# Kernel optimization log

Hardware: AMD Instinct MI355X
Metric: run time of the kernel (lower is better)

## Reference

```python
import jax, jax.numpy as jnp
import numpy as np

# Static problem dims (match input_specs / init_kwargs)
B, NQ, C, H = 2, 900, 256, 8
HGT, WID = 64, 64            # single-scale feature map (input_spatial_shapes = [[64, 64]])
N = HGT * WID                # 4096 keys
DH = C // H                  # head dim 32
RPE_HID = 512
STRIDE = 16                  # feature_stride


def setup_inputs() -> dict:
    key = jax.random.key(0)
    ks = jax.random.split(key, 24)
    p = lambda k, shape: jax.random.normal(k, shape, jnp.float32) * 0.02
    # reference boxes (cx, cy, w, h) in pixel coords of a 1024x1024 image
    ref = jax.random.uniform(ks[0], (B, NQ, 1, 4), jnp.float32)
    ref = jnp.concatenate([ref[..., :2] * (WID * STRIDE), ref[..., 2:] * 128.0], axis=-1)
    return {
        "vggt_features": jnp.zeros((1,), jnp.float32),  # unused by forward (kept for signature fidelity)
        "query": jax.random.normal(ks[1], (B, NQ, C), jnp.float32),
        "reference_2d": ref,
        "k_input_flatten": jax.random.normal(ks[2], (B, N, C), jnp.float32),
        "v_input_flatten": jax.random.normal(ks[3], (B, N, C), jnp.float32),
        "input_spatial_shapes": jnp.array([[HGT, WID]], jnp.int32),
        "input_padding_mask": jnp.zeros((B, N), jnp.bool_),
        # cpb_mlp1 (x) and cpb_mlp2 (y): Linear(2,512)+ReLU+Linear(512,H,no bias); stored as [in,out]
        "W1x": p(ks[4], (2, RPE_HID)), "b1x": jnp.zeros((RPE_HID,), jnp.float32), "W2x": p(ks[5], (RPE_HID, H)),
        "W1y": p(ks[6], (2, RPE_HID)), "b1y": jnp.zeros((RPE_HID,), jnp.float32), "W2y": p(ks[7], (RPE_HID, H)),
        "Wq": p(ks[8], (C, C)), "bq": jnp.zeros((C,), jnp.float32),
        "Wk": p(ks[9], (C, C)), "bk": jnp.zeros((C,), jnp.float32),
        "Wv": p(ks[10], (C, C)), "bv": jnp.zeros((C,), jnp.float32),
        "Wp": p(ks[11], (C, C)), "bp": jnp.zeros((C,), jnp.float32),
    }


def _mlp(d, W1, b1, W2):
    return jax.nn.relu(d @ W1 + b1) @ W2


def reference(vggt_features, query, reference_2d, k_input_flatten, v_input_flatten,
              input_spatial_shapes, input_padding_mask,
              W1x, b1x, W2x, W1y, b1y, W2y, Wq, bq, Wk, bk, Wv, bv, Wp, bp):
    h, w = HGT, WID  # static (input_spatial_shapes[0] == [HGT, WID])
    scale = DH ** -0.5
    # cxcywh -> xyxy: [B, NQ, 1, 4]
    xyxy = jnp.concatenate([reference_2d[..., :2] - reference_2d[..., 2:] / 2,
                            reference_2d[..., :2] + reference_2d[..., 2:] / 2], axis=-1)
    # pixel-center grid coords (linspace(0.5, w-0.5, w) * stride)
    pos_x = ((jnp.arange(w, dtype=jnp.float32) + 0.5) * STRIDE)[None, None, :, None]
    pos_y = ((jnp.arange(h, dtype=jnp.float32) + 0.5) * STRIDE)[None, None, :, None]
    delta_x = xyxy[..., 0::2] - pos_x  # [B, NQ, w, 2]  (x1, x2 rel. to columns)
    delta_y = xyxy[..., 1::2] - pos_y  # [B, NQ, h, 2]  (y1, y2 rel. to rows)
    rpe_x = _mlp(delta_x, W1x, b1x, W2x)  # [B, NQ, w, H]
    rpe_y = _mlp(delta_y, W1y, b1y, W2y)  # [B, NQ, h, H]
    # broadcast add over (row, col) then flatten spatial -> [B, H, NQ, N]
    rpe = (rpe_x[:, :, None] + rpe_y[:, :, :, None]).reshape(B, NQ, h * w, H).transpose(0, 3, 1, 2)
    q = (query @ Wq + bq).reshape(B, NQ, H, DH).transpose(0, 2, 1, 3) * scale  # [B,H,NQ,DH]
    k = (k_input_flatten @ Wk + bk).reshape(B, N, H, DH).transpose(0, 2, 1, 3)  # [B,H,N,DH]
    v = (v_input_flatten @ Wv + bv).reshape(B, N, H, DH).transpose(0, 2, 1, 3)  # [B,H,N,DH]
    attn = jnp.einsum('bhqd,bhkd->bhqk', q, k) + rpe
    attn = attn + input_padding_mask[:, None, None, :].astype(attn.dtype) * (-100.0)
    # torch.clip_ to finfo(min,max) is an identity on finite values; softmax follows
    attn = jax.nn.softmax(attn, axis=-1)
    x = jnp.einsum('bhqk,bhkd->bhqd', attn, v).transpose(0, 2, 1, 3).reshape(B, NQ, C)
    return x @ Wp + bp
```

## Files before the change

### kernel.cpp

```cpp
#include <hip/hip_runtime.h>
#include <hip/hip_bf16.h>
#include <cmath>

#define B_ 2
#define NQ_ 900
#define N_ 4096
#define LOG2E 1.4426950408889634f

typedef __attribute__((ext_vector_type(4))) float f32x4;
typedef __attribute__((ext_vector_type(8))) short s16x8;
typedef __attribute__((ext_vector_type(8))) _Float16 f16x8;

__device__ inline short f2bf(float x) {
    union { __hip_bfloat16 b; short s; } u;
    u.b = __float2bfloat16(x);
    return u.s;
}
__device__ inline short f2h(float x) {
    _Float16 h = (_Float16)x;
    return __builtin_bit_cast(short, h);
}

template <int CTRL>
__device__ inline float dppf(float x) {
    int xi = __builtin_bit_cast(int, x);
    int r = __builtin_amdgcn_update_dpp(xi, xi, CTRL, 0xF, 0xF, true);
    return __builtin_bit_cast(float, r);
}
__device__ inline float rowmax16(float v) {
    v = fmaxf(v, dppf<0x121>(v));
    v = fmaxf(v, dppf<0x122>(v));
    v = fmaxf(v, dppf<0x124>(v));
    v = fmaxf(v, dppf<0x128>(v));
    return v;
}
__device__ inline float rowsum16(float v) {
    v += dppf<0x121>(v);
    v += dppf<0x122>(v);
    v += dppf<0x124>(v);
    v += dppf<0x128>(v);
    return v;
}

__global__ __launch_bounds__(256) void proj_kernel(
    const float* __restrict__ query, const float* __restrict__ kin,
    const float* __restrict__ vin,
    const float* __restrict__ Wq, const float* __restrict__ Wk,
    const float* __restrict__ Wv,
    const float* __restrict__ bqv, const float* __restrict__ bkv,
    const float* __restrict__ bvv,
    unsigned short* __restrict__ qbf, unsigned short* __restrict__ kbf,
    unsigned short* __restrict__ vbf, float qscale)
{
    const int mtx = blockIdx.z;
    const float* X = mtx == 0 ? query : mtx == 1 ? kin : vin;
    const float* W = mtx == 0 ? Wq : mtx == 1 ? Wk : Wv;
    const float* bias = mtx == 0 ? bqv : mtx == 1 ? bkv : bvv;
    unsigned short* Y = mtx == 0 ? qbf : mtx == 1 ? kbf : vbf;
    const int M = mtx == 0 ? 1800 : 8192;
    const int m0 = blockIdx.x * 64;
    if (m0 >= M) return;
    const float alpha = mtx == 0 ? qscale : 1.0f;
    const int rows_per_b = mtx == 0 ? 900 : 4096;
    const int ROWS = mtx == 0 ? 960 : 4096;

    __shared__ short Ab[16384];
    __shared__ short Bb[16384];
    const int tid = threadIdx.x;
    const int w = tid >> 6, l = tid & 63, quad = l >> 4, l15 = l & 15;
    const int wq = tid & 3, mm = tid >> 2;

    {
        const bool valid = (m0 + mm) < M;
        const float* xr = X + (size_t)(m0 + mm) * 256;
        #pragma unroll
        for (int it = 0; it < 8; ++it) {
            int g2 = it * 4 + wq;
            float4 a0 = make_float4(0.f, 0.f, 0.f, 0.f), a1 = a0;
            if (valid) {
                a0 = *(const float4*)(xr + g2 * 8);
                a1 = *(const float4*)(xr + g2 * 8 + 4);
            }
            uint4 pk;
            pk.x = (unsigned)(unsigned short)f2bf(a0.x) | ((unsigned)(unsigned short)f2bf(a0.y) << 16);
            pk.y = (unsigned)(unsigned short)f2bf(a0.z) | ((unsigned)(unsigned short)f2bf(a0.w) << 16);
            pk.z = (unsigned)(unsigned short)f2bf(a1.x) | ((unsigned)(unsigned short)f2bf(a1.y) << 16);
            pk.w = (unsigned)(unsigned short)f2bf(a1.z) | ((unsigned)(unsigned short)f2bf(a1.w) << 16);
            *(uint4*)(Ab + (it * 256 + mm * 4 + wq) * 8) = pk;
        }
    }

    for (int nt0 = 0; nt0 < 4; ++nt0) {
        const int n0 = nt0 * 64;
        {
            const float* wcol = W + n0 + mm;
            #pragma unroll
            for (int it = 0; it < 8; ++it) {
                int g2 = it * 4 + wq;
                uint4 wk4;
                wk4.x = (unsigned)(unsigned short)f2bf(wcol[(g2 * 8 + 0) * 256])
                      | ((unsigned)(unsigned short)f2bf(wcol[(g2 * 8 + 1) * 256]) << 16);
                wk4.y = (unsigned)(unsigned short)f2bf(wcol[(g2 * 8 + 2) * 256])
                      | ((unsigned)(unsigned short)f2bf(wcol[(g2 * 8 + 3) * 256]) << 16);
                wk4.z = (unsigned)(unsigned short)f2bf(wcol[(g2 * 8 + 4) * 256])
                      | ((unsigned)(unsigned short)f2bf(wcol[(g2 * 8 + 5) * 256]) << 16);
                wk4.w = (unsigned)(unsigned short)f2bf(wcol[(g2 * 8 + 6) * 256])
                      | ((unsigned)(unsigned short)f2bf(wcol[(g2 * 8 + 7) * 256]) << 16);
                *(uint4*)(Bb + (it * 256 + mm * 4 + wq) * 8) = wk4;
            }
        }
        __syncthreads();

        f32x4 acc[4] = {{0.f,0.f,0.f,0.f},{0.f,0.f,0.f,0.f},{0.f,0.f,0.f,0.f},{0.f,0.f,0.f,0.f}};
        #pragma unroll
        for (int kc = 0; kc < 8; ++kc) {
            s16x8 a = *(const s16x8*)(Ab + (kc * 256 + (w * 16 + l15) * 4 + quad) * 8);
            #pragma unroll
            for (int nt = 0; nt < 4; ++nt) {
                s16x8 bf = *(const s16x8*)(Bb + (kc * 256 + (nt * 16 + l15) * 4 + quad) * 8);
                acc[nt] = __builtin_amdgcn_mfma_f32_16x16x32_bf16(a, bf, acc[nt], 0, 0, 0);
            }
        }
        __syncthreads();

        #pragma unroll
        for (int nt = 0; nt < 4; ++nt) {
            int n = n0 + nt * 16 + l15;
            float bs = bias[n];
            int h = n >> 5, d = n & 31;
            #pragma unroll
            for (int r = 0; r < 4; ++r) {
                int row = m0 + w * 16 + quad * 4 + r;
                if (row < M) {
                    int b = row / rows_per_b;
                    int pos = row - b * rows_per_b;
                    Y[((size_t)(b * 8 + h) * ROWS + pos) * 32 + d] =
                        (unsigned short)f2bf((acc[nt][r] + bs) * alpha);
                }
            }
        }
    }
}

__global__ __launch_bounds__(256) void outproj_kernel(
    const float* __restrict__ X, const float* __restrict__ W,
    const float* __restrict__ bias, float* __restrict__ Y, int M)
{
    __shared__ short Abh[4096], Abl[4096], Bbh[4096], Bbl[4096];
    const int tid = threadIdx.x;
    const int m0 = blockIdx.x * 64, n0 = blockIdx.y * 64;
    const int w = tid >> 6, l = tid & 63, quad = l >> 4, l15 = l & 15;
    const int wq = tid & 3, mm = tid >> 2;
    const bool valid = (m0 + mm) < M;
    const float* xr = X + (size_t)(m0 + mm) * 256;
    const float* wcol = W + n0 + mm;

    f32x4 acc[4] = {{0.f,0.f,0.f,0.f},{0.f,0.f,0.f,0.f},{0.f,0.f,0.f,0.f},{0.f,0.f,0.f,0.f}};

    for (int kq = 0; kq < 4; ++kq) {
        #pragma unroll
        for (int it = 0; it < 2; ++it) {
            int g2 = it * 4 + wq;
            int kbase = kq * 64 + g2 * 8;
            float av[8], bv[8];
            #pragma unroll
            for (int j = 0; j < 8; ++j) {
                av[j] = valid ? xr[kbase + j] : 0.f;
                bv[j] = wcol[(kbase + j) * 256];
            }
            uint4 ah, al, bh, bl;
            unsigned* ahp = (unsigned*)&ah; unsigned* alp = (unsigned*)&al;
            unsigned* bhp = (unsigned*)&bh; unsigned* blp = (unsigned*)&bl;
            #pragma unroll
            for (int j2 = 0; j2 < 4; ++j2) {
                _Float16 h0 = (_Float16)av[j2 * 2], h1 = (_Float16)av[j2 * 2 + 1];
                ahp[j2] = (unsigned)(unsigned short)__builtin_bit_cast(short, h0)
                        | ((unsigned)(unsigned short)__builtin_bit_cast(short, h1) << 16);
                alp[j2] = (unsigned)(unsigned short)f2h(av[j2 * 2] - (float)h0)
                        | ((unsigned)(unsigned short)f2h(av[j2 * 2 + 1] - (float)h1) << 16);
                _Float16 g0 = (_Float16)bv[j2 * 2], g1 = (_Float16)bv[j2 * 2 + 1];
                bhp[j2] = (unsigned)(unsigned short)__builtin_bit_cast(short, g0)
                        | ((unsigned)(unsigned short)__builtin_bit_cast(short, g1) << 16);
                blp[j2] = (unsigned)(unsigned short)f2h(bv[j2 * 2] - (float)g0)
                        | ((unsigned)(unsigned short)f2h(bv[j2 * 2 + 1] - (float)g1) << 16);
            }
            int gi = (it * 256 + mm * 4 + wq) * 8;
            *(uint4*)(Abh + gi) = ah;
            *(uint4*)(Abl + gi) = al;
            *(uint4*)(Bbh + gi) = bh;
            *(uint4*)(Bbl + gi) = bl;
        }
        __syncthreads();

        #pragma unroll
        for (int kc = 0; kc < 2; ++kc) {
            int ga = (kc * 256 + (w * 16 + l15) * 4 + quad) * 8;
            f16x8 ah = *(const f16x8*)(Abh + ga);
            f16x8 al = *(const f16x8*)(Abl + ga);
            #pragma unroll
            for (int nt = 0; nt < 4; ++nt) {
                int gb = (kc * 256 + (nt * 16 + l15) * 4 + quad) * 8;
                f16x8 bh = *(const f16x8*)(Bbh + gb);
                f16x8 bl = *(const f16x8*)(Bbl + gb);
                acc[nt] = __builtin_amdgcn_mfma_f32_16x16x32_f16(ah, bh, acc[nt], 0, 0, 0);
                acc[nt] = __builtin_amdgcn_mfma_f32_16x16x32_f16(ah, bl, acc[nt], 0, 0, 0);
                acc[nt] = __builtin_amdgcn_mfma_f32_16x16x32_f16(al, bh, acc[nt], 0, 0, 0);
            }
        }
        __syncthreads();
    }

    #pragma unroll
    for (int nt = 0; nt < 4; ++nt) {
        int n = n0 + nt * 16 + l15;
        float bs = bias[n];
        #pragma unroll
        for (int r = 0; r < 4; ++r) {
            int row = m0 + w * 16 + quad * 4 + r;
            if (row < M)
                Y[(size_t)row * 256 + n] = acc[nt][r] + bs;
        }
    }
}

__global__ __launch_bounds__(512) void rpe3_kernel(
    const float* __restrict__ ref2d,
    const float* __restrict__ W1x, const float* __restrict__ b1x,
    const float* __restrict__ W1y, const float* __restrict__ b1y,
    const float* __restrict__ W2x, const float* __restrict__ W2y,
    float* __restrict__ rpe_x, float* __restrict__ rpe_y)
{
    __shared__ short sw2h[8192], sw2l[8192];
    __shared__ float4 sUV[2 * 576];

    const int tid = threadIdx.x;
    for (int i = tid; i < 8192; i += 512) {
        int g = i >> 3, j = i & 7;
        int kcg = g >> 6, rr = g & 63, n = rr >> 2, q4 = rr & 3;
        int k = kcg * 32 + q4 * 8 + j;
        float val = ((n < 8) ? W2x[k * 8 + n] : W2y[k * 8 + (n - 8)]) * LOG2E;
        _Float16 hi = (_Float16)val;
        sw2h[i] = __builtin_bit_cast(short, hi);
        sw2l[i] = f2h(val - (float)hi);
    }
    {
        int k = tid;
        float w1x0 = W1x[k], w1x1 = W1x[512 + k];
        float w1y0 = W1y[k], w1y1 = W1y[512 + k];
        float bx = b1x[k], by = b1y[k];
        float vx = -(w1x0 + w1x1), vy = -(w1y0 + w1y1);
        #pragma unroll
        for (int q2 = 0; q2 < 2; ++q2) {
            const float4 bb = *(const float4*)(ref2d + (size_t)(blockIdx.x * 2 + q2) * 4);
            float ux = fmaf(w1x0, bb.x - bb.z * 0.5f, fmaf(w1x1, bb.x + bb.z * 0.5f, bx));
            float uy = fmaf(w1y0, bb.y - bb.w * 0.5f, fmaf(w1y1, bb.y + bb.w * 0.5f, by));
            sUV[q2 * 576 + (k >> 3) * 9 + (k & 7)] = make_float4(ux, vx, uy, vy);
        }
    }

    const int w = tid >> 6, l = tid & 63, quad = l >> 4, l15 = l & 15;
    const int qi = w >> 2, wrow = w & 3;
    const int bq = blockIdx.x * 2 + qi;
    const int row = wrow * 16 + l15;
    const float pc = (row + 0.5f) * 16.0f;

    __syncthreads();

    f32x4 accx = {0.f, 0.f, 0.f, 0.f}, accy = {0.f, 0.f, 0.f, 0.f};
    for (int kc = 0; kc < 16; ++kc) {
        f16x8 axh, axl, ayh, ayl;
        #pragma unroll
        for (int i = 0; i < 8; ++i) {
            float4 u = sUV[qi * 576 + (kc * 4 + quad) * 9 + i];
            float hx = fmaxf(fmaf(u.y, pc, u.x), 0.f);
            float hy = fmaxf(fmaf(u.w, pc, u.z), 0.f);
            _Float16 xh = (_Float16)hx;
            _Float16 yh = (_Float16)hy;
            axh[i] = xh;
            axl[i] = (_Float16)(hx - (float)xh);
            ayh[i] = yh;
            ayl[i] = (_Float16)(hy - (float)yh);
        }
        f16x8 bh = *(const f16x8*)(sw2h + (kc * 64 + l15 * 4 + quad) * 8);
        f16x8 bl = *(const f16x8*)(sw2l + (kc * 64 + l15 * 4 + quad) * 8);
        accx = __builtin_amdgcn_mfma_f32_16x16x32_f16(axh, bh, accx, 0, 0, 0);
        accx = __builtin_amdgcn_mfma_f32_16x16x32_f16(axh, bl, accx, 0, 0, 0);
        accx = __builtin_amdgcn_mfma_f32_16x16x32_f16(axl, bh, accx, 0, 0, 0);
        accy = __builtin_amdgcn_mfma_f32_16x16x32_f16(ayh, bh, accy, 0, 0, 0);
        accy = __builtin_amdgcn_mfma_f32_16x16x32_f16(ayh, bl, accy, 0, 0, 0);
        accy = __builtin_amdgcn_mfma_f32_16x16x32_f16(ayl, bh, accy, 0, 0, 0);
    }

    #pragma unroll
    for (int rr = 0; rr < 4; ++rr) {
        int row_out = wrow * 16 + quad * 4 + rr;
        if (l15 < 8) rpe_x[((size_t)l15 * 1800 + bq) * 64 + row_out] = accx[rr];
        else         rpe_y[((size_t)(l15 - 8) * 1800 + bq) * 64 + row_out] = accy[rr];
    }
}

__global__ __launch_bounds__(512, 4) void attn_mfma_kernel(
    const unsigned short* __restrict__ qb16, const unsigned short* __restrict__ kb16,
    const unsigned short* __restrict__ vb16,
    const float* __restrict__ rpe_x, const float* __restrict__ rpe_y,
    const unsigned char* __restrict__ mask, float* __restrict__ xout)
{
    __shared__ short skf[4 * 2048];
    __shared__ short svt[4 * 2048];
    __shared__ short spb[8 * 544];
    __shared__ float ry[32 * 65];
    __shared__ unsigned long long smaskb[64];
    __shared__ float sm[8][16], sl[8][16], sLf[32];

    const int tid = threadIdx.x;
    const int qb = blockIdx.x, h = blockIdx.y, b = blockIdx.z;
    const int q0 = qb * 32;
    const int w = tid >> 6, l = tid & 63;
    const int qsub = w >> 2, g = w & 3;
    const int quad = l >> 4, l15 = l & 15;

    const unsigned short* qg = qb16 + (size_t)(b * 8 + h) * 960 * 32;
    const unsigned short* kg = kb16 + (size_t)(b * 8 + h) * 4096 * 32;
    const unsigned short* vg = vb16 + (size_t)(b * 8 + h) * 4096 * 32;
    const float* rxh = rpe_x + ((size_t)h * 1800 + b * NQ_) * 64;
    const float* ryh = rpe_y + ((size_t)h * 1800 + b * NQ_) * 64;

    for (int i = tid; i < 2048; i += 512) {
        int qq = q0 + (i >> 6), pos = i & 63;
        float vy = 0.f;
        if (qq < NQ_)
            vy = ryh[(size_t)qq * 64 + pos];
        ry[(i >> 6) * 65 + pos] = vy;
    }
    #pragma unroll
    for (int j = 0; j < 8; ++j) {
        int c = w * 8 + j;
        unsigned long long bits = __ballot(mask[(size_t)b * N_ + c * 64 + l] != 0);
        if (l == 0) smaskb[c] = bits;
    }

    s16x8 qa = *(const s16x8*)(qg + (size_t)(q0 + qsub * 16 + l15) * 32 + quad * 8);

    f32x4 rx4[4];
    #pragma unroll
    for (int t = 0; t < 4; ++t)
        #pragma unroll
        for (int r = 0; r < 4; ++r) {
            int qq = q0 + qsub * 16 + quad * 4 + r;
            rx4[t][r] = (qq < NQ_) ? rxh[(size_t)qq * 64 + t * 16 + l15] : 0.f;
        }

    const int sg = tid >> 7, role = (tid >> 6) & 1, stl = tid & 63;
    int eoff[4];
    if (role == 0) {
        #pragma unroll
        for (int t = 0; t < 4; ++t)
            eoff[t] = (t * 16 + (stl & 15)) * 32 + (stl >> 4) * 8;
    } else {
        #pragma unroll
        for (int t = 0; t < 4; ++t)
            eoff[t] = stl * 32 + t * 8;
    }
    const unsigned short* src = role ? vg : kg;

    uint4 pf[4];
    {
        size_t cb = (size_t)(sg * 16) * 2048;
        #pragma unroll
        for (int t = 0; t < 4; ++t) pf[t] = *(const uint4*)(src + cb + eoff[t]);
    }

    float mrow[4] = {-INFINITY, -INFINITY, -INFINITY, -INFINITY};
    float lrow[4] = {0.f, 0.f, 0.f, 0.f};
    f32x4 acc0 = {0.f, 0.f, 0.f, 0.f}, acc1 = {0.f, 0.f, 0.f, 0.f};
    short* pw = spb + w * 544;

    for (int i = 0; i < 16; ++i) {
        __syncthreads();
        if (role == 0) {
            #pragma unroll
            for (int t = 0; t < 4; ++t)
                *(uint4*)(skf + sg * 2048 + (t * 64 + stl) * 8) = pf[t];
        } else {
            short* vtw = svt + sg * 2048;
            #pragma unroll
            for (int t = 0; t < 4; ++t) {
                const unsigned short* pv = (const unsigned short*)&pf[t];
                #pragma unroll
                for (int j = 0; j < 8; ++j) {
                    int d = t * 8 + j;
                    vtw[d * 64 + (((stl >> 3) ^ (d & 7)) << 3) + (stl & 7)] = (short)pv[j];
                }
            }
        }
        __syncthreads();

        {
            int inext = (i + 1 < 16) ? i + 1 : 15;
            size_t cb = (size_t)(sg * 16 + inext) * 2048;
            #pragma unroll
            for (int t = 0; t < 4; ++t) pf[t] = *(const uint4*)(src + cb + eoff[t]);
        }

        const int cgc = g * 16 + i;
        const short* kf = skf + g * 2048;

        f32x4 sc[4];
        #pragma unroll
        for (int t = 0; t < 4; ++t) {
            s16x8 kb = *(const s16x8*)(kf + (t * 64 + l) * 8);
            sc[t] = __builtin_amdgcn_mfma_f32_16x16x32_bf16(qa, kb, rx4[t], 0, 0, 0);
        }
        float ryv[4];
        #pragma unroll
        for (int r = 0; r < 4; ++r)
            ryv[r] = ry[(qsub * 16 + quad * 4 + r) * 65 + cgc];
        unsigned long long mb = smaskb[cgc];
        if (mb) {
            #pragma unroll
            for (int t = 0; t < 4; ++t) {
                float mk = ((mb >> (t * 16 + l15)) & 1ULL) ? -144.2695f : 0.f;
                #pragma unroll
                for (int r = 0; r < 4; ++r) sc[t][r] += mk;
            }
        }

        float cmr[4];
        #pragma unroll
        for (int r = 0; r < 4; ++r)
            cmr[r] = fmaxf(fmaxf(sc[0][r], sc[1][r]), fmaxf(sc[2][r], sc[3][r])) + ryv[r];

        int ok = (cmr[0] <= mrow[0] + 8.f) & (cmr[1] <= mrow[1] + 8.f)
               & (cmr[2] <= mrow[2] + 8.f) & (cmr[3] <= mrow[3] + 8.f);
        if (!__all(ok)) {
            #pragma unroll
            for (int r = 0; r < 4; ++r) {
                float cm = rowmax16(cmr[r]);
                float mnew = fmaxf(mrow[r], cm);
                float al = exp2f(mrow[r] - mnew);
                mrow[r] = mnew;
                lrow[r] *= al;
                acc0[r] *= al;
                acc1[r] *= al;
            }
        }

        float msub[4];
        #pragma unroll
        for (int r = 0; r < 4; ++r) msub[r] = mrow[r] - ryv[r];
        #pragma unroll
        for (int t = 0; t < 4; ++t)
            #pragma unroll
            for (int r = 0; r < 4; ++r)
                sc[t][r] = exp2f(sc[t][r] - msub[r]);
        #pragma unroll
        for (int r = 0; r < 4; ++r)
            lrow[r] += (sc[0][r] + sc[1][r]) + (sc[2][r] + sc[3][r]);

        const short* vt = svt + g * 2048;
        #pragma unroll
        for (int hh = 0; hh < 2; ++hh) {
            #pragma unroll
            for (int tt = 0; tt < 2; ++tt) {
                int t = hh * 2 + tt;
                int gphys = (tt * 2 + (l15 >> 3)) ^ quad;
                #pragma unroll
                for (int r = 0; r < 4; ++r)
                    pw[(gphys * 17 + quad * 4 + r) * 8 + (l15 & 7)] = f2bf(sc[t][r]);
            }
            int gph_r = quad ^ (l15 >> 2);
            s16x8 pa  = *(const s16x8*)(pw + (gph_r * 17 + l15) * 8);
            int ksw = ((hh * 4 + quad) ^ (l15 & 7)) * 8;
            s16x8 vb0 = *(const s16x8*)(vt + l15 * 64 + ksw);
            s16x8 vb1 = *(const s16x8*)(vt + (16 + l15) * 64 + ksw);
            acc0 = __builtin_amdgcn_mfma_f32_16x16x32_bf16(pa, vb0, acc0, 0, 0, 0);
            acc1 = __builtin_amdgcn_mfma_f32_16x16x32_bf16(pa, vb1, acc1, 0, 0, 0);
        }
    }

    #pragma unroll
    for (int r = 0; r < 4; ++r) lrow[r] = rowsum16(lrow[r]);

    __syncthreads();
    if (l15 == 0) {
        #pragma unroll
        for (int r = 0; r < 4; ++r) {
            sm[w][quad * 4 + r] = mrow[r];
            sl[w][quad * 4 + r] = lrow[r];
        }
    }
    __syncthreads();
    float wgt[4], L4[4];
    #pragma unroll
    for (int r = 0; r < 4; ++r) {
        int qrow = quad * 4 + r;
        float mm = -INFINITY;
        #pragma unroll
        for (int gg = 0; gg < 4; ++gg) mm = fmaxf(mm, sm[qsub * 4 + gg][qrow]);
        float LL = 0.f;
        #pragma unroll
        for (int gg = 0; gg < 4; ++gg)
            LL += exp2f(sm[qsub * 4 + gg][qrow] - mm) * sl[qsub * 4 + gg][qrow];
        wgt[r] = exp2f(mrow[r] - mm);
        L4[r] = LL;
    }
    if (g == 0 && l15 == 0) {
        #pragma unroll
        for (int r = 0; r < 4; ++r) sLf[qsub * 16 + quad * 4 + r] = L4[r];
    }

    float* obuf = (float*)skf;
    for (int gg = 0; gg < 4; ++gg) {
        if (g == gg) {
            #pragma unroll
            for (int r = 0; r < 4; ++r) {
                int idx = (qsub * 16 + quad * 4 + r) * 33 + l15;
                float v0 = wgt[r] * acc0[r];
                float v1 = wgt[r] * acc1[r];
                if (gg == 0) { obuf[idx] = v0; obuf[idx + 16] = v1; }
                else         { obuf[idx] += v0; obuf[idx + 16] += v1; }
            }
        }
        __syncthreads();
    }

    for (int i = tid; i < 1024; i += 512) {
        int ql = i >> 5, d = i & 31;
        int qq = q0 + ql;
        if (qq < NQ_)
            xout[(size_t)(b * NQ_ + qq) * 256 + h * 32 + d] = obuf[ql * 33 + d] / sLf[ql];
    }
}

extern "C" void kernel_launch(void* const* d_in, const int* in_sizes, int n_in,
                              void* d_out, int out_size, void* d_ws, size_t ws_size,
                              hipStream_t stream)
{
    const float* query = (const float*)d_in[1];
    const float* ref2d = (const float*)d_in[2];
    const float* kin   = (const float*)d_in[3];
    const float* vin   = (const float*)d_in[4];
    const unsigned char* mask = (const unsigned char*)d_in[6];
    const float* W1x = (const float*)d_in[7];
    const float* b1x = (const float*)d_in[8];
    const float* W2x = (const float*)d_in[9];
    const float* W1y = (const float*)d_in[10];
    const float* b1y = (const float*)d_in[11];
    const float* W2y = (const float*)d_in[12];
    const float* Wq  = (const float*)d_in[13];
    const float* bq  = (const float*)d_in[14];
    const float* Wk  = (const float*)d_in[15];
    const float* bk  = (const float*)d_in[16];
    const float* Wv  = (const float*)d_in[17];
    const float* bv  = (const float*)d_in[18];
    const float* Wp  = (const float*)d_in[19];
    const float* bp  = (const float*)d_in[20];

    char* wsb = (char*)d_ws;
    unsigned short* qbf = (unsigned short*)(wsb);
    unsigned short* kbf = (unsigned short*)(wsb +   983040);
    unsigned short* vbf = (unsigned short*)(wsb +  5177344);
    float* rxws = (float*)(wsb +  9371648);
    float* ryws = (float*)(wsb + 13058048);
    float* xws  = (float*)(wsb + 16744448);
    float* out  = (float*)d_out;

    const float qscale = LOG2E / sqrtf(32.0f);

    proj_kernel<<<dim3(128, 1, 3), 256, 0, stream>>>(
        query, kin, vin, Wq, Wk, Wv, bq, bk, bv, qbf, kbf, vbf, qscale);
    rpe3_kernel<<<900, 512, 0, stream>>>(
        ref2d, W1x, b1x, W1y, b1y, W2x, W2y, rxws, ryws);
    attn_mfma_kernel<<<dim3(29, 8, B_), 512, 0, stream>>>(
        qbf, kbf, vbf, rxws, ryws, mask, xws);
    outproj_kernel<<<dim3(29, 4), 256, 0, stream>>>(xws, Wp, bp, out, 1800);
}
```

Baseline: 232.6 us.

## Merge QKV projection and RPE MLP into one heterogeneous stage-1 kernel

Combines the QKV projection and the RPE MLP kernels into a single launch whose blocks branch on blockIdx: the first 285 blocks do projection tiles (dead blocks from the old padded grid are gone) and the remaining 1800 blocks each compute the RPE for one query. The projection weight tile is now staged in two K-halves, halving its shared memory so the union buffer fits 48KB and more blocks can be resident. This removes one kernel launch and lets the two independent stages overlap on the GPU. In exchange it adds extra syncs in the projection loop, and each RPE block now reloads the W2 tables for a single query instead of two.

Measured after the change: 218.0 us. 6.3% less time.

```diff
diff --git a/kernel.cpp b/kernel.cpp
--- a/kernel.cpp
+++ b/kernel.cpp
@@ -42,7 +42,7 @@
     return v;
 }
 
-__global__ __launch_bounds__(256) void proj_kernel(
+__global__ __launch_bounds__(256) void stage1_kernel(
     const float* __restrict__ query, const float* __restrict__ kin,
     const float* __restrict__ vin,
     const float* __restrict__ Wq, const float* __restrict__ Wk,
@@ -50,94 +50,170 @@
     const float* __restrict__ bqv, const float* __restrict__ bkv,
     const float* __restrict__ bvv,
     unsigned short* __restrict__ qbf, unsigned short* __restrict__ kbf,
-    unsigned short* __restrict__ vbf, float qscale)
+    unsigned short* __restrict__ vbf, float qscale,
+    const float* __restrict__ ref2d,
+    const float* __restrict__ W1x, const float* __restrict__ b1x,
+    const float* __restrict__ W1y, const float* __restrict__ b1y,
+    const float* __restrict__ W2x, const float* __restrict__ W2y,
+    float* __restrict__ rpe_x, float* __restrict__ rpe_y)
 {
-    const int mtx = blockIdx.z;
-    const float* X = mtx == 0 ? query : mtx == 1 ? kin : vin;
-    const float* W = mtx == 0 ? Wq : mtx == 1 ? Wk : Wv;
-    const float* bias = mtx == 0 ? bqv : mtx == 1 ? bkv : bvv;
-    unsigned short* Y = mtx == 0 ? qbf : mtx == 1 ? kbf : vbf;
-    const int M = mtx == 0 ? 1800 : 8192;
-    const int m0 = blockIdx.x * 64;
-    if (m0 >= M) return;
-    const float alpha = mtx == 0 ? qscale : 1.0f;
-    const int rows_per_b = mtx == 0 ? 900 : 4096;
-    const int ROWS = mtx == 0 ? 960 : 4096;
-
-    __shared__ short Ab[16384];
-    __shared__ short Bb[16384];
+    __shared__ uint4 smem[3072];
+    const int bx = blockIdx.x;
     const int tid = threadIdx.x;
     const int w = tid >> 6, l = tid & 63, quad = l >> 4, l15 = l & 15;
-    const int wq = tid & 3, mm = tid >> 2;
-
-    {
-        const bool valid = (m0 + mm) < M;
-        const float* xr = X + (size_t)(m0 + mm) * 256;
-        #pragma unroll
-        for (int it = 0; it < 8; ++it) {
-            int g2 = it * 4 + wq;
-            float4 a0 = make_float4(0.f, 0.f, 0.f, 0.f), a1 = a0;
-            if (valid) {
-                a0 = *(const float4*)(xr + g2 * 8);
-                a1 = *(const float4*)(xr + g2 * 8 + 4);
-            }
-            uint4 pk;
-            pk.x = (unsigned)(unsigned short)f2bf(a0.x) | ((unsigned)(unsigned short)f2bf(a0.y) << 16);
-            pk.y = (unsigned)(unsigned short)f2bf(a0.z) | ((unsigned)(unsigned short)f2bf(a0.w) << 16);
-            pk.z = (unsigned)(unsigned short)f2bf(a1.x) | ((unsigned)(unsigned short)f2bf(a1.y) << 16);
-            pk.w = (unsigned)(unsigned short)f2bf(a1.z) | ((unsigned)(unsigned short)f2bf(a1.w) << 16);
-            *(uint4*)(Ab + (it * 256 + mm * 4 + wq) * 8) = pk;
-        }
-    }
-
-    for (int nt0 = 0; nt0 < 4; ++nt0) {
-        const int n0 = nt0 * 64;
+
+    if (bx < 285) {
+        short* Ab = (short*)smem;
+        short* Bb = (short*)smem + 16384;
+        const int mtx = bx < 29 ? 0 : (bx < 157 ? 1 : 2);
+        const int tile = bx - (mtx == 0 ? 0 : mtx == 1 ? 29 : 157);
+        const int m0 = tile * 64;
+        const float* X = mtx == 0 ? query : mtx == 1 ? kin : vin;
+        const float* W = mtx == 0 ? Wq : mtx == 1 ? Wk : Wv;
+        const float* bias = mtx == 0 ? bqv : mtx == 1 ? bkv : bvv;
+        unsigned short* Y = mtx == 0 ? qbf : mtx == 1 ? kbf : vbf;
+        const int M = mtx == 0 ? 1800 : 8192;
+        const float alpha = mtx == 0 ? qscale : 1.0f;
+        const int rows_per_b = mtx == 0 ? 900 : 4096;
+        const int ROWS = mtx == 0 ? 960 : 4096;
+        const int wq = tid & 3, mm = tid >> 2;
+
         {
-            const float* wcol = W + n0 + mm;
+            const bool valid = (m0 + mm) < M;
+            const float* xr = X + (size_t)(m0 + mm) * 256;
             #pragma unroll
             for (int it = 0; it < 8; ++it) {
                 int g2 = it * 4 + wq;
-                uint4 wk4;
-                wk4.x = (unsigned)(unsigned short)f2bf(wcol[(g2 * 8 + 0) * 256])
-                      | ((unsigned)(unsigned short)f2bf(wcol[(g2 * 8 + 1) * 256]) << 16);
-                wk4.y = (unsigned)(unsigned short)f2bf(wcol[(g2 * 8 + 2) * 256])
-                      | ((unsigned)(unsigned short)f2bf(wcol[(g2 * 8 + 3) * 256]) << 16);
-                wk4.z = (unsigned)(unsigned short)f2bf(wcol[(g2 * 8 + 4) * 256])
-                      | ((unsigned)(unsigned short)f2bf(wcol[(g2 * 8 + 5) * 256]) << 16);
-                wk4.w = (unsigned)(unsigned short)f2bf(wcol[(g2 * 8 + 6) * 256])
-                      | ((unsigned)(unsigned short)f2bf(wcol[(g2 * 8 + 7) * 256]) << 16);
-                *(uint4*)(Bb + (it * 256 + mm * 4 + wq) * 8) = wk4;
-            }
-        }
+                float4 a0 = make_float4(0.f, 0.f, 0.f, 0.f), a1 = a0;
+                if (valid) {
+                    a0 = *(const float4*)(xr + g2 * 8);
+                    a1 = *(const float4*)(xr + g2 * 8 + 4);
+                }
+                uint4 pk;
+                pk.x = (unsigned)(unsigned short)f2bf(a0.x) | ((unsigned)(unsigned short)f2bf(a0.y) << 16);
+                pk.y = (unsigned)(unsigned short)f2bf(a0.z) | ((unsigned)(unsigned short)f2bf(a0.w) << 16);
+                pk.z = (unsigned)(unsigned short)f2bf(a1.x) | ((unsigned)(unsigned short)f2bf(a1.y) << 16);
+                pk.w = (unsigned)(unsigned short)f2bf(a1.z) | ((unsigned)(unsigned short)f2bf(a1.w) << 16);
+                *(uint4*)(Ab + (it * 256 + mm * 4 + wq) * 8) = pk;
+            }
+        }
+
+        for (int nt0 = 0; nt0 < 4; ++nt0) {
+            const int n0 = nt0 * 64;
+            f32x4 acc[4] = {{0.f,0.f,0.f,0.f},{0.f,0.f,0.f,0.f},{0.f,0.f,0.f,0.f},{0.f,0.f,0.f,0.f}};
+            for (int kh = 0; kh < 2; ++kh) {
+                {
+                    const float* wcol = W + n0 + mm;
+                    #pragma unroll
+                    for (int it = 0; it < 4; ++it) {
+                        int g2 = it * 4 + wq;
+                        int kb = kh * 128 + g2 * 8;
+                        uint4 wk4;
+                        wk4.x = (unsigned)(unsigned short)f2bf(wcol[(kb + 0) * 256])
+                              | ((unsigned)(unsigned short)f2bf(wcol[(kb + 1) * 256]) << 16);
+                        wk4.y = (unsigned)(unsigned short)f2bf(wcol[(kb + 2) * 256])
+                              | ((unsigned)(unsigned short)f2bf(wcol[(kb + 3) * 256]) << 16);
+                        wk4.z = (unsigned)(unsigned short)f2bf(wcol[(kb + 4) * 256])
+                              | ((unsigned)(unsigned short)f2bf(wcol[(kb + 5) * 256]) << 16);
+                        wk4.w = (unsigned)(unsigned short)f2bf(wcol[(kb + 6) * 256])
+                              | ((unsigned)(unsigned short)f2bf(wcol[(kb + 7) * 256]) << 16);
+                        *(uint4*)(Bb + (it * 256 + mm * 4 + wq) * 8) = wk4;
+                    }
+                }
+                __syncthreads();
+
+                #pragma unroll
+                for (int kc = 0; kc < 4; ++kc) {
+                    int kcg = kh * 4 + kc;
+                    s16x8 a = *(const s16x8*)(Ab + (kcg * 256 + (w * 16 + l15) * 4 + quad) * 8);
+                    #pragma unroll
+                    for (int nt = 0; nt < 4; ++nt) {
+                        s16x8 bf = *(const s16x8*)(Bb + (kc * 256 + (nt * 16 + l15) * 4 + quad) * 8);
+                        acc[nt] = __builtin_amdgcn_mfma_f32_16x16x32_bf16(a, bf, acc[nt], 0, 0, 0);
+                    }
+                }
+                __syncthreads();
+            }
+
+            #pragma unroll
+            for (int nt = 0; nt < 4; ++nt) {
+                int n = n0 + nt * 16 + l15;
+                float bs = bias[n];
+                int h = n >> 5, d = n & 31;
+                #pragma unroll
+                for (int r = 0; r < 4; ++r) {
+                    int row = m0 + w * 16 + quad * 4 + r;
+                    if (row < M) {
+                        int b = row / rows_per_b;
+                        int pos = row - b * rows_per_b;
+                        Y[((size_t)(b * 8 + h) * ROWS + pos) * 32 + d] =
+                            (unsigned short)f2bf((acc[nt][r] + bs) * alpha);
+                    }
+                }
+            }
+        }
+    } else {
+        short* sw2h = (short*)smem;
+        short* sw2l = (short*)smem + 8192;
+        float4* sUV = (float4*)(smem + 2048);
+        const int bq = bx - 285;
+
+        for (int i = tid; i < 8192; i += 256) {
+            int g = i >> 3, j = i & 7;
+            int kcg = g >> 6, rr = g & 63, n = rr >> 2, q4 = rr & 3;
+            int k = kcg * 32 + q4 * 8 + j;
+            float val = ((n < 8) ? W2x[k * 8 + n] : W2y[k * 8 + (n - 8)]) * LOG2E;
+            _Float16 hi = (_Float16)val;
+            sw2h[i] = __builtin_bit_cast(short, hi);
+            sw2l[i] = f2h(val - (float)hi);
+        }
+        for (int k = tid; k < 512; k += 256) {
+            float w1x0 = W1x[k], w1x1 = W1x[512 + k];
+            float w1y0 = W1y[k], w1y1 = W1y[512 + k];
+            float bxv = b1x[k], byv = b1y[k];
+            float vx = -(w1x0 + w1x1), vy = -(w1y0 + w1y1);
+            const float4 bb = *(const float4*)(ref2d + (size_t)bq * 4);
+            float ux = fmaf(w1x0, bb.x - bb.z * 0.5f, fmaf(w1x1, bb.x + bb.z * 0.5f, bxv));
+            float uy = fmaf(w1y0, bb.y - bb.w * 0.5f, fmaf(w1y1, bb.y + bb.w * 0.5f, byv));
+            sUV[(k >> 3) * 9 + (k & 7)] = make_float4(ux, vx, uy, vy);
+        }
+
+        const int wrow = w;
+        const int row = wrow * 16 + l15;
+        const float pc = (row + 0.5f) * 16.0f;
+
         __syncthreads();
 
-        f32x4 acc[4] = {{0.f,0.f,0.f,0.f},{0.f,0.f,0.f,0.f},{0.f,0.f,0.f,0.f},{0.f,0.f,0.f,0.f}};
-        #pragma unroll
-        for (int kc = 0; kc < 8; ++kc) {
-            s16x8 a = *(const s16x8*)(Ab + (kc * 256 + (w * 16 + l15) * 4 + quad) * 8);
-            #pragma unroll
-            for (int nt = 0; nt < 4; ++nt) {
-                s16x8 bf = *(const s16x8*)(Bb + (kc * 256 + (nt * 16 + l15) * 4 + quad) * 8);
-                acc[nt] = __builtin_amdgcn_mfma_f32_16x16x32_bf16(a, bf, acc[nt], 0, 0, 0);
-            }
-        }
-        __syncthreads();
-
-        #pragma unroll
-        for (int nt = 0; nt < 4; ++nt) {
-            int n = n0 + nt * 16 + l15;
-            float bs = bias[n];
-            int h = n >> 5, d = n & 31;
-            #pragma unroll
-            for (int r = 0; r < 4; ++r) {
-                int row = m0 + w * 16 + quad * 4 + r;
-                if (row < M) {
-                    int b = row / rows_per_b;
-                    int pos = row - b * rows_per_b;
-                    Y[((size_t)(b * 8 + h) * ROWS + pos) * 32 + d] =
-                        (unsigned short)f2bf((acc[nt][r] + bs) * alpha);
-                }
-            }
+        f32x4 accx = {0.f, 0.f, 0.f, 0.f}, accy = {0.f, 0.f, 0.f, 0.f};
+        for (int kc = 0; kc < 16; ++kc) {
+            f16x8 axh, axl, ayh, ayl;
+            #pragma unroll
+            for (int i = 0; i < 8; ++i) {
+                float4 u = sUV[(kc * 4 + quad) * 9 + i];
+                float hx = fmaxf(fmaf(u.y, pc, u.x), 0.f);
+                float hy = fmaxf(fmaf(u.w, pc, u.z), 0.f);
+                _Float16 xh = (_Float16)hx;
+                _Float16 yh = (_Float16)hy;
+                axh[i] = xh;
+                axl[i] = (_Float16)(hx - (float)xh);
+                ayh[i] = yh;
+                ayl[i] = (_Float16)(hy - (float)yh);
+            }
+            f16x8 bh = *(const f16x8*)(sw2h + (kc * 64 + l15 * 4 + quad) * 8);
+            f16x8 bl = *(const f16x8*)(sw2l + (kc * 64 + l15 * 4 + quad) * 8);
+            accx = __builtin_amdgcn_mfma_f32_16x16x32_f16(axh, bh, accx, 0, 0, 0);
+            accx = __builtin_amdgcn_mfma_f32_16x16x32_f16(axh, bl, accx, 0, 0, 0);
+            accx = __builtin_amdgcn_mfma_f32_16x16x32_f16(axl, bh, accx, 0, 0, 0);
+            accy = __builtin_amdgcn_mfma_f32_16x16x32_f16(ayh, bh, accy, 0, 0, 0);
+            accy = __builtin_amdgcn_mfma_f32_16x16x32_f16(ayh, bl, accy, 0, 0, 0);
+            accy = __builtin_amdgcn_mfma_f32_16x16x32_f16(ayl, bh, accy, 0, 0, 0);
+        }
+
+        #pragma unroll
+        for (int rr = 0; rr < 4; ++rr) {
+            int row_out = wrow * 16 + quad * 4 + rr;
+            if (l15 < 8) rpe_x[((size_t)l15 * 1800 + bq) * 64 + row_out] = accx[rr];
+            else         rpe_y[((size_t)(l15 - 8) * 1800 + bq) * 64 + row_out] = accy[rr];
         }
     }
 }
@@ -220,82 +296,6 @@
             if (row < M)
                 Y[(size_t)row * 256 + n] = acc[nt][r] + bs;
         }
-    }
-}
-
-__global__ __launch_bounds__(512) void rpe3_kernel(
-    const float* __restrict__ ref2d,
-    const float* __restrict__ W1x, const float* __restrict__ b1x,
-    const float* __restrict__ W1y, const float* __restrict__ b1y,
-    const float* __restrict__ W2x, const float* __restrict__ W2y,
-    float* __restrict__ rpe_x, float* __restrict__ rpe_y)
-{
-    __shared__ short sw2h[8192], sw2l[8192];
-    __shared__ float4 sUV[2 * 576];
-
-    const int tid = threadIdx.x;
-    for (int i = tid; i < 8192; i += 512) {
-        int g = i >> 3, j = i & 7;
-        int kcg = g >> 6, rr = g & 63, n = rr >> 2, q4 = rr & 3;
-        int k = kcg * 32 + q4 * 8 + j;
-        float val = ((n < 8) ? W2x[k * 8 + n] : W2y[k * 8 + (n - 8)]) * LOG2E;
-        _Float16 hi = (_Float16)val;
-        sw2h[i] = __builtin_bit_cast(short, hi);
-        sw2l[i] = f2h(val - (float)hi);
-    }
-    {
-        int k = tid;
-        float w1x0 = W1x[k], w1x1 = W1x[512 + k];
-        float w1y0 = W1y[k], w1y1 = W1y[512 + k];
-        float bx = b1x[k], by = b1y[k];
-        float vx = -(w1x0 + w1x1), vy = -(w1y0 + w1y1);
-        #pragma unroll
-        for (int q2 = 0; q2 < 2; ++q2) {
-            const float4 bb = *(const float4*)(ref2d + (size_t)(blockIdx.x * 2 + q2) * 4);
-            float ux = fmaf(w1x0, bb.x - bb.z * 0.5f, fmaf(w1x1, bb.x + bb.z * 0.5f, bx));
-            float uy = fmaf(w1y0, bb.y - bb.w * 0.5f, fmaf(w1y1, bb.y + bb.w * 0.5f, by));
-            sUV[q2 * 576 + (k >> 3) * 9 + (k & 7)] = make_float4(ux, vx, uy, vy);
-        }
-    }
-
-    const int w = tid >> 6, l = tid & 63, quad = l >> 4, l15 = l & 15;
-    const int qi = w >> 2, wrow = w & 3;
-    const int bq = blockIdx.x * 2 + qi;
-    const int row = wrow * 16 + l15;
-    const float pc = (row + 0.5f) * 16.0f;
-
-    __syncthreads();
-
-    f32x4 accx = {0.f, 0.f, 0.f, 0.f}, accy = {0.f, 0.f, 0.f, 0.f};
-    for (int kc = 0; kc < 16; ++kc) {
-        f16x8 axh, axl, ayh, ayl;
-        #pragma unroll
-        for (int i = 0; i < 8; ++i) {
-            float4 u = sUV[qi * 576 + (kc * 4 + quad) * 9 + i];
-            float hx = fmaxf(fmaf(u.y, pc, u.x), 0.f);
-            float hy = fmaxf(fmaf(u.w, pc, u.z), 0.f);
-            _Float16 xh = (_Float16)hx;
-            _Float16 yh = (_Float16)hy;
-            axh[i] = xh;
-            axl[i] = (_Float16)(hx - (float)xh);
-            ayh[i] = yh;
-            ayl[i] = (_Float16)(hy - (float)yh);
-        }
-        f16x8 bh = *(const f16x8*)(sw2h + (kc * 64 + l15 * 4 + quad) * 8);
-        f16x8 bl = *(const f16x8*)(sw2l + (kc * 64 + l15 * 4 + quad) * 8);
-        accx = __builtin_amdgcn_mfma_f32_16x16x32_f16(axh, bh, accx, 0, 0, 0);
-        accx = __builtin_amdgcn_mfma_f32_16x16x32_f16(axh, bl, accx, 0, 0, 0);
-        accx = __builtin_amdgcn_mfma_f32_16x16x32_f16(axl, bh, accx, 0, 0, 0);
-        accy = __builtin_amdgcn_mfma_f32_16x16x32_f16(ayh, bh, accy, 0, 0, 0);
-        accy = __builtin_amdgcn_mfma_f32_16x16x32_f16(ayh, bl, accy, 0, 0, 0);
-        accy = __builtin_amdgcn_mfma_f32_16x16x32_f16(ayl, bh, accy, 0, 0, 0);
-    }
-
-    #pragma unroll
-    for (int rr = 0; rr < 4; ++rr) {
-        int row_out = wrow * 16 + quad * 4 + rr;
-        if (l15 < 8) rpe_x[((size_t)l15 * 1800 + bq) * 64 + row_out] = accx[rr];
-        else         rpe_y[((size_t)(l15 - 8) * 1800 + bq) * 64 + row_out] = accy[rr];
     }
 }
 
@@ -567,9 +567,8 @@
 
     const float qscale = LOG2E / sqrtf(32.0f);
 
-    proj_kernel<<<dim3(128, 1, 3), 256, 0, stream>>>(
-        query, kin, vin, Wq, Wk, Wv, bq, bk, bv, qbf, kbf, vbf, qscale);
-    rpe3_kernel<<<900, 512, 0, stream>>>(
+    stage1_kernel<<<2085, 256, 0, stream>>>(
+        query, kin, vin, Wq, Wk, Wv, bq, bk, bv, qbf, kbf, vbf, qscale,
         ref2d, W1x, b1x, W1y, b1y, W2x, W2y, rxws, ryws);
     attn_mfma_kernel<<<dim3(29, 8, B_), 512, 0, stream>>>(
         qbf, kbf, vbf, rxws, ryws, mask, xws);
```
